# Kernel tuning notes

Measured on AMD Instinct MI355X. Metric: run time of the kernel, lower is better.

Reference implementation:

```python
import jax, jax.numpy as jnp
import numpy as np

KSIZE = 7
SIGMA = 1.5
VIS_THRESH = 0.1


def _gaussian_kernel1d(ks, sigma):
    xs = jnp.linspace(-(ks - 1) / 2.0, (ks - 1) / 2.0, ks)
    k = jnp.exp(-0.5 * (xs / sigma) ** 2)
    return k / k.sum()


def setup_inputs() -> dict:
    key = jax.random.key(0)
    k1, k2 = jax.random.split(key)
    x = jax.random.normal(k1, (8, 32, 256, 256), dtype=jnp.float32)
    urnd = jax.random.uniform(k2, (5, 8, 32, 256, 256), dtype=jnp.float32)
    return {"x": x, "urnd": urnd}


def reference(x, urnd):
    b, c, h, w = x.shape
    T = urnd.shape[0]  # sampling_times
    s = jax.nn.sigmoid(x)                       # [b,c,h,w]
    crnd = s[None] * urnd                       # [T,b,c,h,w]
    flat = crnd.reshape(T, b, c, h * w)
    arg = jnp.argmax(flat, axis=-1)             # [T,b,c]
    mx = jnp.max(flat, axis=-1)                 # value at argmax location
    ii = (arg // w).astype(s.dtype) / h
    jj = (arg % w).astype(s.dtype) / w
    joints = jnp.stack([ii, jj], axis=-1)       # [T,b,c,2]
    # row=round(ii*h), col=round(jj*w) recover exactly the argmax location,
    # so the visibility check is crnd[argmax] >= 0.1, i.e. mx >= 0.1.
    vis_t = mx >= VIS_THRESH                    # [T,b,c]
    joints = jnp.where(vis_t[..., None], joints, 0.0)
    m_joints = joints.mean(axis=0)              # [b,c,2]
    v_joints = joints.var(axis=0, ddof=1)       # torch.var unbiased default
    vis = vis_t.astype(s.dtype).mean(axis=0) > 0.5  # [b,c] bool
    m_joints = jnp.where(vis[..., None], m_joints, 0.0)
    v_joints = jnp.where(vis[..., None], v_joints, 0.0)
    # scatter single point per (b,c) where visible
    rows = jnp.clip(jnp.round(m_joints[..., 0] * h).astype(jnp.int32), 0, h - 1)
    cols = jnp.clip(jnp.round(m_joints[..., 1] * w).astype(jnp.int32), 0, w - 1)
    idx = rows * w + cols                       # [b,c]
    bb = jnp.arange(b)[:, None]
    cc = jnp.arange(c)[None, :]
    vals = jnp.where(vis, jnp.asarray(1.0, s.dtype), jnp.asarray(0.0, s.dtype))
    att = jnp.zeros((b, c, h * w), s.dtype).at[bb, cc, idx].set(vals)
    att = att.reshape(b, c, h, w)
    # Gaussian blur 7x7, sigma=1.5, reflect padding (torchvision GaussianBlur)
    k1 = _gaussian_kernel1d(KSIZE, SIGMA).astype(s.dtype)
    kern = (k1[:, None] * k1[None, :])[None, None]  # [1,1,7,7]
    pad = KSIZE // 2
    ap = jnp.pad(att.reshape(b * c, 1, h, w),
                 ((0, 0), (0, 0), (pad, pad), (pad, pad)), mode='reflect')
    att = jax.lax.conv_general_dilated(
        ap, kern, (1, 1), 'VALID',
        dimension_numbers=('NCHW', 'OIHW', 'NCHW')).reshape(b, c, h, w)
    att = (att - att.min()) / (att.max() - att.min())
    return att, m_joints, v_joints, vis
```

## Files before the change

### kernel.cpp

```cpp
#include <hip/hip_runtime.h>
#include <math.h>

#define NT 5
#define NB 8
#define NC 32
#define NH 256
#define NW 256
#define NHW (NH * NW)
#define NBC (NB * NC)
#define NTBC (NT * NBC)
#define KS 7
#define PAD 3
#define VIS_TH 0.1f

#define QRT 4
#define NUNITS (NTBC * QRT)
#define EPQ (NHW / QRT)
#define V4PQ (EPQ / 4)
#define ITER (V4PQ / 256)

typedef float vf4 __attribute__((ext_vector_type(4)));


__device__ __forceinline__ void make_k1(float k[KS]) {
    float s = 0.f;
#pragma unroll
    for (int i = 0; i < KS; ++i) {
        float xx = (float)i - 3.0f;
        float t = xx / 1.5f;
        k[i] = expf(-0.5f * t * t);
        s += k[i];
    }
    float inv = 1.0f / s;
#pragma unroll
    for (int i = 0; i < KS; ++i) k[i] *= inv;
}

__device__ __forceinline__ int refl(int z) {
    z = (z < 0) ? -z : z;
    z = (z >= NH) ? (2 * NH - 2 - z) : z;
    return z;
}

__device__ __forceinline__ float rweight(int y, int r, const float k1[KS]) {
    float s = 0.f;
#pragma unroll
    for (int d = 0; d < KS; ++d) {
        int z = y + d - PAD;
        if (refl(z) == r) s += k1[d];
    }
    return s;
}

__device__ __forceinline__ float rwmax(int r, const float k1[KS]) {
    float m = 0.f;
#pragma unroll
    for (int y = 0; y < KS; ++y) m = fmaxf(m, rweight(y, r, k1));
    int lo = max(0, r - PAD), hi = min(NH - 1, r + PAD);
    for (int y = lo; y <= hi; ++y) m = fmaxf(m, rweight(y, r, k1));
#pragma unroll
    for (int y = NH - KS; y < NH; ++y) m = fmaxf(m, rweight(y, r, k1));
    return m;
}


__global__ __launch_bounds__(256, 4) void k_argmax(
        const float* __restrict__ x, const float* __restrict__ urnd,
        float* __restrict__ pmx, int* __restrict__ parg) {
    const int tid = threadIdx.x;
    const int bc = blockIdx.x >> 2;
    const int q = blockIdx.x & (QRT - 1);

    const vf4* x4 = (const vf4*)x + (size_t)bc * (NHW / 4) + q * V4PQ;
    const vf4* u4 = (const vf4*)urnd + (size_t)bc * (NHW / 4) + q * V4PQ;
    const size_t TS = (size_t)NBC * (NHW / 4);

    float bt[NT];
    int it[NT];
#pragma unroll
    for (int t = 0; t < NT; ++t) { bt[t] = -1.f; it[t] = 0; }

#pragma unroll 2
    for (int j = 0; j < ITER; ++j) {
        const int v = j * 256 + tid;
        vf4 xx = __builtin_nontemporal_load(x4 + v);
        const float s0 = 1.f / (1.f + expf(-xx[0]));
        const float s1 = 1.f / (1.f + expf(-xx[1]));
        const float s2 = 1.f / (1.f + expf(-xx[2]));
        const float s3 = 1.f / (1.f + expf(-xx[3]));
        const int base = v * 4;
#pragma unroll
        for (int t = 0; t < NT; ++t) {
            vf4 uu = __builtin_nontemporal_load(u4 + (size_t)t * TS + v);
            float p0 = s0 * uu[0], p1 = s1 * uu[1];
            float p2 = s2 * uu[2], p3 = s3 * uu[3];
            if (p0 > bt[t]) { bt[t] = p0; it[t] = base; }
            if (p1 > bt[t]) { bt[t] = p1; it[t] = base + 1; }
            if (p2 > bt[t]) { bt[t] = p2; it[t] = base + 2; }
            if (p3 > bt[t]) { bt[t] = p3; it[t] = base + 3; }
        }
    }

#pragma unroll
    for (int t = 0; t < NT; ++t) {
        float best = bt[t];
        int bidx = it[t];
#pragma unroll
        for (int m = 32; m; m >>= 1) {
            float ov = __shfl_xor(best, m, 64);
            int oi = __shfl_xor(bidx, m, 64);
            if (ov > best || (ov == best && oi < bidx)) { best = ov; bidx = oi; }
        }
        bt[t] = best;
        it[t] = bidx;
    }

    __shared__ float sv[NT][4];
    __shared__ int si[NT][4];
    const int w = tid >> 6;
    if ((tid & 63) == 0) {
#pragma unroll
        for (int t = 0; t < NT; ++t) { sv[t][w] = bt[t]; si[t][w] = it[t]; }
    }
    __syncthreads();
    if (tid < NT) {
        float best = sv[tid][0];
        int bidx = si[tid][0];
#pragma unroll
        for (int ww = 1; ww < 4; ++ww) {
            if (sv[tid][ww] > best || (sv[tid][ww] == best && si[tid][ww] < bidx)) {
                best = sv[tid][ww];
                bidx = si[tid][ww];
            }
        }
        pmx[(tid * NBC + bc) * QRT + q] = best;
        parg[(tid * NBC + bc) * QRT + q] = q * EPQ + bidx;
    }
}


__global__ __launch_bounds__(256, 4) void k_statt(
        const float* __restrict__ pmx, const int* __restrict__ parg,
        float* __restrict__ out_m, float* __restrict__ out_v,
        float* __restrict__ out_vis, float* __restrict__ att) {
    const int tid = threadIdx.x;
    const int myc = blockIdx.x >> 2;
    const int qy = blockIdx.x & 3;

    float k1[KS];
    make_k1(k1);

    float ji[NT], jj[NT];
    int visn = 0;
#pragma unroll
    for (int t = 0; t < NT; ++t) {
        int u0 = (t * NBC + tid) * QRT;
        float m = pmx[u0]; int a = parg[u0];
#pragma unroll
        for (int q = 1; q < QRT; ++q) {
            float mq = pmx[u0 + q];
            if (mq > m) { m = mq; a = parg[u0 + q]; }
        }
        bool vt = (m >= VIS_TH);
        float ii = (float)(a >> 8) * (1.0f / (float)NH);
        float jv = (float)(a & (NW - 1)) * (1.0f / (float)NW);
        ji[t] = vt ? ii : 0.f;
        jj[t] = vt ? jv : 0.f;
        visn += vt ? 1 : 0;
    }
    float mi = (ji[0] + ji[1] + ji[2] + ji[3] + ji[4]) / 5.0f;
    float mj = (jj[0] + jj[1] + jj[2] + jj[3] + jj[4]) / 5.0f;
    float vi = 0.f, vj = 0.f;
#pragma unroll
    for (int t = 0; t < NT; ++t) {
        float di = ji[t] - mi, dj = jj[t] - mj;
        vi += di * di;
        vj += dj * dj;
    }
    vi /= (float)(NT - 1);
    vj /= (float)(NT - 1);

    bool vis = (visn >= 3);

    if (blockIdx.x == 0) {
        out_m[tid * 2 + 0] = vis ? mi : 0.f;
        out_m[tid * 2 + 1] = vis ? mj : 0.f;
        out_v[tid * 2 + 0] = vis ? vi : 0.f;
        out_v[tid * 2 + 1] = vis ? vj : 0.f;
        out_vis[tid] = vis ? 1.f : 0.f;
    }

    int r = min(max((int)roundf((vis ? mi : 0.f) * (float)NH), 0), NH - 1);
    int c = min(max((int)roundf((vis ? mj : 0.f) * (float)NW), 0), NW - 1);
    float cmax = vis ? (rwmax(r, k1) * rwmax(c, k1)) : 0.f;

    __shared__ int sR[NBC], sC[NBC], sVis[NBC];
    __shared__ float sG[NBC];
    sR[tid] = r; sC[tid] = c; sVis[tid] = vis ? 1 : 0; sG[tid] = cmax;
    __syncthreads();
#pragma unroll
    for (int off = 128; off; off >>= 1) {
        if (tid < off) sG[tid] = fmaxf(sG[tid], sG[tid + off]);
        __syncthreads();
    }
    const float gmax = sG[0];
    const int r_ = sR[myc], c_ = sC[myc], vis_ = sVis[myc];

    vf4* out4 = (vf4*)(att + (size_t)myc * NHW) + qy * (NHW / 4 / 4);

    if (!vis_) {
        vf4 z = {0.f, 0.f, 0.f, 0.f};
#pragma unroll
        for (int j = 0; j < 16; ++j)
            __builtin_nontemporal_store(z, out4 + j * 256 + tid);
        return;
    }

    __shared__ float sRW[64];
    if (tid < 64) sRW[tid] = rweight(qy * 64 + tid, r_, k1);
    const int xq = tid & 63;
    const float cw0 = rweight(4 * xq + 0, c_, k1);
    const float cw1 = rweight(4 * xq + 1, c_, k1);
    const float cw2 = rweight(4 * xq + 2, c_, k1);
    const float cw3 = rweight(4 * xq + 3, c_, k1);
    __syncthreads();

    const int w = tid >> 6;
#pragma unroll
    for (int j = 0; j < 16; ++j) {
        float rw = sRW[j * 4 + w];
        vf4 o;
        if (rw == 0.f) {
            o = (vf4){0.f, 0.f, 0.f, 0.f};
        } else {
            float r0 = rw * cw0, r1 = rw * cw1, r2 = rw * cw2, r3 = rw * cw3;
            o[0] = (r0 == 0.f) ? 0.f : (r0 / gmax);
            o[1] = (r1 == 0.f) ? 0.f : (r1 / gmax);
            o[2] = (r2 == 0.f) ? 0.f : (r2 / gmax);
            o[3] = (r3 == 0.f) ? 0.f : (r3 / gmax);
        }
        __builtin_nontemporal_store(o, out4 + j * 256 + tid);
    }
}


extern "C" void kernel_launch(void* const* d_in, const int* in_sizes, int n_in,
                              void* d_out, int out_size, void* d_ws, size_t ws_size,
                              hipStream_t stream) {
    const float* x = (const float*)d_in[0];
    const float* urnd = (const float*)d_in[1];

    float* out = (float*)d_out;
    float* out_att = out;
    float* out_m = out + (size_t)NBC * NHW;
    float* out_v = out_m + NBC * 2;
    float* out_vis = out_v + NBC * 2;

    char* ws = (char*)d_ws;
    float* pmx = (float*)ws;                ws += NUNITS * sizeof(float);
    int* parg = (int*)ws;

    k_argmax<<<NBC * QRT, 256, 0, stream>>>(x, urnd, pmx, parg);
    k_statt<<<NBC * 4, 256, 0, stream>>>(pmx, parg, out_m, out_v, out_vis, out_att);
}
```

Baseline: 83.69 us.

## Stage sigmoid chunks in LDS and stream each sampling plane sequentially

The argmax kernel now computes sigmoid for an 8192-element chunk into shared memory, then walks each of the five urnd planes over that chunk in turn, instead of reading all five planes at once per element. The intent is more sequential, better-pipelined memory streams per plane with deeper unrolling. In exchange it adds 32KB of LDS per block, which limits occupancy, plus two barriers per chunk and LDS round trips.

```diff
diff --git a/kernel.cpp b/kernel.cpp
--- a/kernel.cpp
+++ b/kernel.cpp
@@ -16,8 +16,10 @@
 #define QRT 4
 #define NUNITS (NTBC * QRT)
 #define EPQ (NHW / QRT)
-#define V4PQ (EPQ / 4)
-#define ITER (V4PQ / 256)
+#define CHUNK_E 8192
+#define CHUNK_V4 (CHUNK_E / 4)
+#define JITER (CHUNK_V4 / 256)
+#define NCHUNK (EPQ / CHUNK_E)
 
 typedef float vf4 __attribute__((ext_vector_type(4)));
 
@@ -71,34 +73,53 @@
     const int bc = blockIdx.x >> 2;
     const int q = blockIdx.x & (QRT - 1);
 
-    const vf4* x4 = (const vf4*)x + (size_t)bc * (NHW / 4) + q * V4PQ;
-    const vf4* u4 = (const vf4*)urnd + (size_t)bc * (NHW / 4) + q * V4PQ;
+    const vf4* x4 = (const vf4*)x + (size_t)bc * (NHW / 4) + q * (EPQ / 4);
+    const vf4* u4 = (const vf4*)urnd + (size_t)bc * (NHW / 4) + q * (EPQ / 4);
     const size_t TS = (size_t)NBC * (NHW / 4);
+
+    __shared__ __align__(16) float sSig[CHUNK_E];
+    vf4* sS4 = (vf4*)sSig;
 
     float bt[NT];
     int it[NT];
 #pragma unroll
     for (int t = 0; t < NT; ++t) { bt[t] = -1.f; it[t] = 0; }
 
-#pragma unroll 2
-    for (int j = 0; j < ITER; ++j) {
-        const int v = j * 256 + tid;
-        vf4 xx = __builtin_nontemporal_load(x4 + v);
-        const float s0 = 1.f / (1.f + expf(-xx[0]));
-        const float s1 = 1.f / (1.f + expf(-xx[1]));
-        const float s2 = 1.f / (1.f + expf(-xx[2]));
-        const float s3 = 1.f / (1.f + expf(-xx[3]));
-        const int base = v * 4;
+    for (int ch = 0; ch < NCHUNK; ++ch) {
+        const int cb4 = ch * CHUNK_V4;
+        const int cbe = ch * CHUNK_E;
+
+#pragma unroll 4
+        for (int k = 0; k < JITER; ++k) {
+            const int v = k * 256 + tid;
+            vf4 xx = __builtin_nontemporal_load(x4 + cb4 + v);
+            vf4 ss;
+            ss[0] = 1.f / (1.f + expf(-xx[0]));
+            ss[1] = 1.f / (1.f + expf(-xx[1]));
+            ss[2] = 1.f / (1.f + expf(-xx[2]));
+            ss[3] = 1.f / (1.f + expf(-xx[3]));
+            sS4[v] = ss;
+        }
+        __syncthreads();
+
 #pragma unroll
         for (int t = 0; t < NT; ++t) {
-            vf4 uu = __builtin_nontemporal_load(u4 + (size_t)t * TS + v);
-            float p0 = s0 * uu[0], p1 = s1 * uu[1];
-            float p2 = s2 * uu[2], p3 = s3 * uu[3];
-            if (p0 > bt[t]) { bt[t] = p0; it[t] = base; }
-            if (p1 > bt[t]) { bt[t] = p1; it[t] = base + 1; }
-            if (p2 > bt[t]) { bt[t] = p2; it[t] = base + 2; }
-            if (p3 > bt[t]) { bt[t] = p3; it[t] = base + 3; }
-        }
+            const vf4* ut = u4 + (size_t)t * TS + cb4;
+#pragma unroll 4
+            for (int j = 0; j < JITER; ++j) {
+                const int v = j * 256 + tid;
+                vf4 uu = __builtin_nontemporal_load(ut + v);
+                vf4 ss = sS4[v];
+                float p0 = ss[0] * uu[0], p1 = ss[1] * uu[1];
+                float p2 = ss[2] * uu[2], p3 = ss[3] * uu[3];
+                const int base = cbe + v * 4;
+                if (p0 > bt[t]) { bt[t] = p0; it[t] = base; }
+                if (p1 > bt[t]) { bt[t] = p1; it[t] = base + 1; }
+                if (p2 > bt[t]) { bt[t] = p2; it[t] = base + 2; }
+                if (p3 > bt[t]) { bt[t] = p3; it[t] = base + 3; }
+            }
+        }
+        __syncthreads();
     }
 
 #pragma unroll
```

Result: no change. 82.91 us (median of 2 runs) (-0.9%).
